# Performance work log

Hardware: AMD Instinct MI355X
Metric: run time of the kernel (lower is better)

Reference implementation:

```python
import jax, jax.numpy as jnp
import numpy as np

B, L, E = 8, 2048, 4096
TOKEN_DIM, EDGE_DIM, HIDDEN = 768, 256, 128


def setup_inputs() -> dict:
    key = jax.random.key(0)
    k1, k2, k3, k4, k5 = jax.random.split(key, 5)
    token_embedding = jax.random.normal(k1, (B, L, TOKEN_DIM), dtype=jnp.float32)
    edge_embedding = jax.random.normal(k2, (B, E, EDGE_DIM), dtype=jnp.float32)
    # fc: Linear(token_dim+edge_dim -> hidden, bias=False); stored as [in, out]
    W_fc = jax.random.normal(k3, (TOKEN_DIM + EDGE_DIM, HIDDEN), dtype=jnp.float32) * 0.02
    # attn_fc: Linear(2*hidden -> 1); weight flattened to [2*hidden], plus scalar bias
    a_attn = jax.random.normal(k4, (2 * HIDDEN,), dtype=jnp.float32) * 0.02
    b_attn = jax.random.normal(k5, (1,), dtype=jnp.float32) * 0.02
    return {"token_embedding": token_embedding, "edge_embedding": edge_embedding,
            "W_fc": W_fc, "a_attn": a_attn, "b_attn": b_attn}


def reference(token_embedding, edge_embedding, W_fc, a_attn, b_attn):
    # avg edge embedding, broadcast over sequence
    avg_edge = edge_embedding.mean(axis=1, keepdims=True)          # [B, 1, De]
    avg_edge = jnp.broadcast_to(avg_edge, (token_embedding.shape[0],
                                           token_embedding.shape[1],
                                           avg_edge.shape[-1]))     # [B, L, De]
    combined = jnp.concatenate([token_embedding, avg_edge], axis=-1)  # [B, L, Dt+De]
    h = jnp.einsum('bld,dh->blh', combined, W_fc)                   # [B, L, H]

    # Additive attention decomposition: a^T [h_j || h_i] = a1.h_j + a2.h_i
    # (original builds concat([h_repeat_row (=h_j), h_repeat_col (=h_i)]))
    H = h.shape[-1]
    a1, a2 = a_attn[:H], a_attn[H:]
    s_j = jnp.einsum('blh,h->bl', h, a1)                            # score contrib from h_j
    s_i = jnp.einsum('blh,h->bl', h, a2)                            # score contrib from h_i
    scores = s_i[:, :, None] + s_j[:, None, :] + b_attn[0]          # [B, L, L], scores[b,i,j]
    attn = jax.nn.softmax(scores, axis=-1)                          # softmax over j
    h_prime = jnp.einsum('bij,bjh->bih', attn, h)                   # [B, L, H]
    return h_prime
```

## Files before the change

kernel.cpp:

```cpp
#include <hip/hip_runtime.h>

constexpr int Bn  = 8;
constexpr int Ln  = 2048;
constexpr int En  = 4096;
constexpr int TDn = 768;
constexpr int EDn = 256;
constexpr int Hn  = 128;

constexpr int OFF_V1    = 0;
constexpr int OFF_DEN   = 768;
constexpr int OFF_T     = 1024;
constexpr int OFF_ES    = 8192;
constexpr int OFF_ROW   = 10240;
constexpr int OFF_EPART = 16384;
constexpr int OFF_TPART = 278528;
constexpr int REC = 772;

__global__ __launch_bounds__(256)
void K_init(const float* __restrict__ W, const float* __restrict__ a,
            float* __restrict__ ws) {
    const int tid = threadIdx.x, wv = tid >> 6, lane = tid & 63;
    int d = blockIdx.x * 4 + wv;
    float acc = W[d * Hn + lane]      * a[lane]
              + W[d * Hn + 64 + lane] * a[64 + lane];
    #pragma unroll
    for (int off = 32; off > 0; off >>= 1)
        acc += __shfl_down(acc, off, 64);
    if (lane == 0) ws[OFF_V1 + d] = acc;
}

__global__ __launch_bounds__(256)
void K_main(const float* __restrict__ token, const float* __restrict__ edge,
            float* __restrict__ ws) {
    const int tid = threadIdx.x, wv = tid >> 6, lane = tid & 63;
    __shared__ float4 s_red[4][64];
    __shared__ float4 s_v1[TDn / 4];
    __shared__ float  s_s[16];
    __shared__ float  s_e[16];

    if (blockIdx.x < 1024) {
        int eb = blockIdx.x;
        int b = eb >> 7, chunk = eb & 127;
        const float4* e4 = (const float4*)edge
                         + ((size_t)(b * En + chunk * 32 + wv * 8)) * (EDn / 4) + lane;
        float4 acc = {0.f, 0.f, 0.f, 0.f};
        #pragma unroll
        for (int i = 0; i < 8; ++i) {
            float4 v = e4[(size_t)i * (EDn / 4)];
            acc.x += v.x; acc.y += v.y; acc.z += v.z; acc.w += v.w;
        }
        s_red[wv][lane] = acc;
        __syncthreads();
        if (tid < 64) {
            float4 r0 = s_red[0][tid], r1 = s_red[1][tid],
                   r2 = s_red[2][tid], r3 = s_red[3][tid];
            float4 s = {r0.x + r1.x + r2.x + r3.x, r0.y + r1.y + r2.y + r3.y,
                        r0.z + r1.z + r2.z + r3.z, r0.w + r1.w + r2.w + r3.w};
            ((float4*)(ws + OFF_EPART))[eb * 64 + tid] = s;
        }
        return;
    }

    int tb = blockIdx.x - 1024;
    const int b = tb >> 7, chunk = tb & 127;
    const size_t row0 = (size_t)(b * Ln + chunk * 16);

    if (tid < TDn / 4) s_v1[tid] = ((const float4*)(ws + OFF_V1))[tid];
    __syncthreads();

    #pragma unroll
    for (int i = 0; i < 4; ++i) {
        int li = wv * 4 + i;
        const float4* t4 = (const float4*)token + (row0 + li) * (TDn / 4);
        float acc = 0.f;
        #pragma unroll
        for (int j = 0; j < 3; ++j) {
            float4 t = t4[lane + 64 * j];
            float4 v = s_v1[lane + 64 * j];
            acc += t.x * v.x + t.y * v.y + t.z * v.z + t.w * v.w;
        }
        #pragma unroll
        for (int off = 32; off > 0; off >>= 1)
            acc += __shfl_down(acc, off, 64);
        if (lane == 0) s_s[li] = acc;
    }
    __syncthreads();

    if (tid < 16) s_e[tid] = expf(s_s[tid]);
    __syncthreads();

    float sum = 0.f;
    #pragma unroll
    for (int l = 0; l < 16; ++l) sum += s_e[l];

    const float* tok = token + row0 * TDn;
    float a0 = 0.f, a1 = 0.f, a2 = 0.f;
    #pragma unroll 4
    for (int l = 0; l < 16; ++l) {
        float e = s_e[l];
        const float* r = tok + (size_t)l * TDn;
        a0 += e * r[tid];
        a1 += e * r[tid + 256];
        a2 += e * r[tid + 512];
    }
    float* rec = ws + OFF_TPART + (size_t)tb * REC;
    if (tid == 0) rec[0] = sum;
    rec[4 + tid]       = a0;
    rec[4 + tid + 256] = a1;
    rec[4 + tid + 512] = a2;
}

__global__ __launch_bounds__(256)
void K2(float* __restrict__ ws) {
    const int tid = threadIdx.x;
    if (blockIdx.x < 24) {
        int b = blockIdx.x / 3, part = blockIdx.x % 3;
        const float* recs = ws + OFF_TPART + (size_t)(b * 128) * REC + 4 + part * 256;
        float acc = 0.f;
        #pragma unroll 4
        for (int k = 0; k < 128; ++k) acc += recs[(size_t)k * REC + tid];
        ws[OFF_T + b * TDn + part * 256 + tid] = acc;
    } else {
        int b = blockIdx.x - 24;
        const float* p = ws + OFF_EPART + (size_t)(b * 128) * EDn + tid;
        float acc = 0.f;
        #pragma unroll 4
        for (int k = 0; k < 128; ++k) acc += p[(size_t)k * EDn];
        ws[OFF_ES + b * EDn + tid] = acc * (1.0f / En);

        __shared__ float s_red[128];
        if (tid < 128)
            s_red[tid] = ws[OFF_TPART + (size_t)(b * 128 + tid) * REC];
        __syncthreads();
        if (tid < 64)  { s_red[tid] += s_red[tid + 64]; } __syncthreads();
        if (tid < 32)  { s_red[tid] += s_red[tid + 32]; } __syncthreads();
        if (tid < 16)  { s_red[tid] += s_red[tid + 16]; } __syncthreads();
        if (tid == 0) {
            float d = 0.f;
            #pragma unroll
            for (int i = 0; i < 16; ++i) d += s_red[i];
            ws[OFF_DEN + b] = d;
        }
    }
}

__global__ __launch_bounds__(256)
void K3(const float* __restrict__ W, float* __restrict__ ws) {
    __shared__ float s_c[1024];
    __shared__ float s_red[256];
    const int b = blockIdx.x >> 3, hg = blockIdx.x & 7;
    const int tid = threadIdx.x;
    const int hidx = tid & 15, dseg = tid >> 4;
    const int h = hg * 16 + hidx;

    float invden = 1.0f / ws[OFF_DEN + b];
    #pragma unroll
    for (int k = 0; k < 4; ++k) {
        int i = tid + k * 256;
        s_c[i] = (i < TDn) ? ws[OFF_T + b * TDn + i] * invden
                           : ws[OFF_ES + b * EDn + (i - TDn)];
    }
    __syncthreads();

    const float* w = W + (dseg * 64) * Hn + h;
    float acc = 0.f;
    #pragma unroll 4
    for (int i = 0; i < 64; ++i)
        acc += s_c[dseg * 64 + i] * w[i * Hn];
    s_red[tid] = acc;
    __syncthreads();
    if (tid < 16) {
        float r = 0.f;
        #pragma unroll
        for (int g = 0; g < 16; ++g) r += s_red[g * 16 + tid];
        ws[OFF_ROW + b * Hn + hg * 16 + tid] = r;
    }
}

__global__ __launch_bounds__(256)
void K4(const float* __restrict__ ws, float4* __restrict__ out) {
    int idx = blockIdx.x * blockDim.x + threadIdx.x;
    int b = idx >> 16;
    int q = idx & (Hn / 4 - 1);
    out[idx] = ((const float4*)(ws + OFF_ROW))[b * (Hn / 4) + q];
}

extern "C" void kernel_launch(void* const* d_in, const int* in_sizes, int n_in,
                              void* d_out, int out_size, void* d_ws, size_t ws_size,
                              hipStream_t stream) {
    const float* token = (const float*)d_in[0];
    const float* edge  = (const float*)d_in[1];
    const float* W     = (const float*)d_in[2];
    const float* a     = (const float*)d_in[3];
    float* ws  = (float*)d_ws;
    float4* out = (float4*)d_out;

    K_init<<<192,  256, 0, stream>>>(W, a, ws);
    K_main<<<2048, 256, 0, stream>>>(token, edge, ws);
    K2    <<<32,   256, 0, stream>>>(ws);
    K3    <<<64,   256, 0, stream>>>(W, ws);
    K4    <<<2048, 256, 0, stream>>>(ws, out);
}
```

Baseline: 138.0 us.

## Fuse all stages into one cooperative kernel with grid-wide syncs

Replaces the five separate kernel launches with a single cooperative kernel of 1024 blocks that runs each stage in turn, separated by grid.sync(). Each block now handles both an edge chunk and a token chunk, and the output broadcast writes two float4 per thread. The aim is to remove launch overhead and inter-kernel gaps. In exchange it adds grid-barrier cost, and stages that only use a few blocks leave most of the grid idle. It falls back to the old multi-kernel path if the cooperative launch fails.

```diff
diff --git a/kernel.cpp b/kernel.cpp
--- a/kernel.cpp
+++ b/kernel.cpp
@@ -1,4 +1,7 @@
 #include <hip/hip_runtime.h>
+#include <hip/hip_cooperative_groups.h>
+
+namespace cg = cooperative_groups;
 
 constexpr int Bn  = 8;
 constexpr int Ln  = 2048;
@@ -15,6 +18,173 @@
 constexpr int OFF_EPART = 16384;
 constexpr int OFF_TPART = 278528;
 constexpr int REC = 772;
+
+__global__ __launch_bounds__(256, 4)
+void K_all(const float* __restrict__ token, const float* __restrict__ edge,
+           const float* __restrict__ W, const float* __restrict__ a,
+           float* __restrict__ ws, float4* __restrict__ out)
+{
+    cg::grid_group grid = cg::this_grid();
+    const int tid = threadIdx.x, wv = tid >> 6, lane = tid & 63;
+    const int bi = blockIdx.x;
+
+    __shared__ __align__(16) float sm[2048];
+
+    if (bi < 192) {
+        int d = bi * 4 + wv;
+        float acc = W[d * Hn + lane]      * a[lane]
+                  + W[d * Hn + 64 + lane] * a[64 + lane];
+        #pragma unroll
+        for (int off = 32; off > 0; off >>= 1)
+            acc += __shfl_down(acc, off, 64);
+        if (lane == 0) ws[OFF_V1 + d] = acc;
+    }
+    grid.sync();
+
+    {
+        const int b = bi >> 7, chunk = bi & 127;
+
+        const float4* e4 = (const float4*)edge
+                         + ((size_t)(b * En + chunk * 32 + wv * 8)) * (EDn / 4) + lane;
+        float4 acc = {0.f, 0.f, 0.f, 0.f};
+        #pragma unroll
+        for (int i = 0; i < 8; ++i) {
+            float4 v = e4[(size_t)i * (EDn / 4)];
+            acc.x += v.x; acc.y += v.y; acc.z += v.z; acc.w += v.w;
+        }
+        float4* RED = (float4*)(sm + 768);
+        RED[wv * 64 + lane] = acc;
+        __syncthreads();
+        if (tid < 64) {
+            float4 r0 = RED[tid], r1 = RED[64 + tid],
+                   r2 = RED[128 + tid], r3 = RED[192 + tid];
+            float4 s = {r0.x + r1.x + r2.x + r3.x, r0.y + r1.y + r2.y + r3.y,
+                        r0.z + r1.z + r2.z + r3.z, r0.w + r1.w + r2.w + r3.w};
+            ((float4*)(ws + OFF_EPART))[bi * 64 + tid] = s;
+        }
+
+        float4* V1 = (float4*)sm;
+        if (tid < TDn / 4) V1[tid] = ((const float4*)(ws + OFF_V1))[tid];
+        __syncthreads();
+
+        const size_t row0 = (size_t)(b * Ln + chunk * 16);
+        float* s_s = sm + 1792;
+        float* s_e = sm + 1808;
+
+        #pragma unroll
+        for (int i = 0; i < 4; ++i) {
+            int li = wv * 4 + i;
+            const float4* t4 = (const float4*)token + (row0 + li) * (TDn / 4);
+            float acc2 = 0.f;
+            #pragma unroll
+            for (int j = 0; j < 3; ++j) {
+                float4 t = t4[lane + 64 * j];
+                float4 v = V1[lane + 64 * j];
+                acc2 += t.x * v.x + t.y * v.y + t.z * v.z + t.w * v.w;
+            }
+            #pragma unroll
+            for (int off = 32; off > 0; off >>= 1)
+                acc2 += __shfl_down(acc2, off, 64);
+            if (lane == 0) s_s[li] = acc2;
+        }
+        __syncthreads();
+        if (tid < 16) s_e[tid] = expf(s_s[tid]);
+        __syncthreads();
+
+        float sum = 0.f;
+        #pragma unroll
+        for (int l = 0; l < 16; ++l) sum += s_e[l];
+
+        const float* tok = token + row0 * TDn;
+        float a0 = 0.f, a1 = 0.f, a2 = 0.f;
+        #pragma unroll 4
+        for (int l = 0; l < 16; ++l) {
+            float e = s_e[l];
+            const float* r = tok + (size_t)l * TDn;
+            a0 += e * r[tid];
+            a1 += e * r[tid + 256];
+            a2 += e * r[tid + 512];
+        }
+        float* rec = ws + OFF_TPART + (size_t)bi * REC;
+        if (tid == 0) rec[0] = sum;
+        rec[4 + tid]       = a0;
+        rec[4 + tid + 256] = a1;
+        rec[4 + tid + 512] = a2;
+    }
+    grid.sync();
+
+    if (bi < 32) {
+        if (bi < 24) {
+            int b = bi / 3, part = bi % 3;
+            const float* recs = ws + OFF_TPART + (size_t)(b * 128) * REC + 4 + part * 256;
+            float acc = 0.f;
+            #pragma unroll 4
+            for (int k = 0; k < 128; ++k) acc += recs[(size_t)k * REC + tid];
+            ws[OFF_T + b * TDn + part * 256 + tid] = acc;
+        } else {
+            int b = bi - 24;
+            const float* p = ws + OFF_EPART + (size_t)(b * 128) * EDn + tid;
+            float acc = 0.f;
+            #pragma unroll 4
+            for (int k = 0; k < 128; ++k) acc += p[(size_t)k * EDn];
+            ws[OFF_ES + b * EDn + tid] = acc * (1.0f / En);
+
+            if (tid < 128)
+                sm[tid] = ws[OFF_TPART + (size_t)(b * 128 + tid) * REC];
+            __syncthreads();
+            if (tid < 64)  { sm[tid] += sm[tid + 64]; } __syncthreads();
+            if (tid < 32)  { sm[tid] += sm[tid + 32]; } __syncthreads();
+            if (tid < 16)  { sm[tid] += sm[tid + 16]; } __syncthreads();
+            if (tid == 0) {
+                float d = 0.f;
+                #pragma unroll
+                for (int i = 0; i < 16; ++i) d += sm[i];
+                ws[OFF_DEN + b] = d;
+            }
+        }
+    }
+    grid.sync();
+
+    if (bi < 64) {
+        float* s_c  = sm;
+        float* s_rd = sm + 1024;
+        const int b = bi >> 3, hg = bi & 7;
+        const int hidx = tid & 15, dseg = tid >> 4;
+        const int h = hg * 16 + hidx;
+
+        float invden = 1.0f / ws[OFF_DEN + b];
+        #pragma unroll
+        for (int k = 0; k < 4; ++k) {
+            int i = tid + k * 256;
+            s_c[i] = (i < TDn) ? ws[OFF_T + b * TDn + i] * invden
+                               : ws[OFF_ES + b * EDn + (i - TDn)];
+        }
+        __syncthreads();
+
+        const float* w = W + (dseg * 64) * Hn + h;
+        float acc = 0.f;
+        #pragma unroll 4
+        for (int i = 0; i < 64; ++i)
+            acc += s_c[dseg * 64 + i] * w[i * Hn];
+        s_rd[tid] = acc;
+        __syncthreads();
+        if (tid < 16) {
+            float r = 0.f;
+            #pragma unroll
+            for (int g = 0; g < 16; ++g) r += s_rd[g * 16 + tid];
+            ws[OFF_ROW + b * Hn + hg * 16 + tid] = r;
+        }
+    }
+    grid.sync();
+
+    {
+        const float4* row4 = (const float4*)(ws + OFF_ROW);
+        int i0 = bi * 512 + tid;
+        out[i0] = row4[(i0 >> 16) * (Hn / 4) + (i0 & (Hn / 4 - 1))];
+        int i1 = i0 + 256;
+        out[i1] = row4[(i1 >> 16) * (Hn / 4) + (i1 & (Hn / 4 - 1))];
+    }
+}
 
 __global__ __launch_bounds__(256)
 void K_init(const float* __restrict__ W, const float* __restrict__ a,
@@ -192,12 +362,18 @@
     const float* edge  = (const float*)d_in[1];
     const float* W     = (const float*)d_in[2];
     const float* a     = (const float*)d_in[3];
-    float* ws  = (float*)d_ws;
+    float* ws   = (float*)d_ws;
     float4* out = (float4*)d_out;
 
-    K_init<<<192,  256, 0, stream>>>(W, a, ws);
-    K_main<<<2048, 256, 0, stream>>>(token, edge, ws);
-    K2    <<<32,   256, 0, stream>>>(ws);
-    K3    <<<64,   256, 0, stream>>>(W, ws);
-    K4    <<<2048, 256, 0, stream>>>(ws, out);
-}
+    void* args[6] = {(void*)&token, (void*)&edge, (void*)&W, (void*)&a,
+                     (void*)&ws, (void*)&out};
+    hipError_t err = hipLaunchCooperativeKernel(K_all, dim3(1024), dim3(256),
+                                                args, 0u, stream);
+    if (err != hipSuccess) {
+        K_init<<<192,  256, 0, stream>>>(W, a, ws);
+        K_main<<<2048, 256, 0, stream>>>(token, edge, ws);
+        K2    <<<32,   256, 0, stream>>>(ws);
+        K3    <<<64,   256, 0, stream>>>(W, ws);
+        K4    <<<2048, 256, 0, stream>>>(ws, out);
+    }
+}
```

Result: slower. 505.6 us (+266.4%).

## Fuse five launches into two, recomputing projection vectors per block

Applied to the files above, without the earlier changes.

Folds the W·a projection into the token-scoring blocks, so every token block recomputes the 768-length vector from W and a in shared memory. The per-batch reductions, the small GEMV and the broadcast write are merged into one second kernel. In that kernel each of 32 slices per batch redundantly re-reduces the partials before writing its share of the output. Token blocks now cover 32 rows instead of 16, halving the partial records. This removes three launches and their inter-kernel gaps, at the cost of much redundant L2 traffic from re-reading W and the partials in every block.

```diff
diff --git a/kernel.cpp b/kernel.cpp
--- a/kernel.cpp
+++ b/kernel.cpp
@@ -7,36 +7,17 @@
 constexpr int EDn = 256;
 constexpr int Hn  = 128;
 
-constexpr int OFF_V1    = 0;
-constexpr int OFF_DEN   = 768;
-constexpr int OFF_T     = 1024;
-constexpr int OFF_ES    = 8192;
-constexpr int OFF_ROW   = 10240;
 constexpr int OFF_EPART = 16384;
 constexpr int OFF_TPART = 278528;
 constexpr int REC = 772;
 
 __global__ __launch_bounds__(256)
-void K_init(const float* __restrict__ W, const float* __restrict__ a,
-            float* __restrict__ ws) {
+void K_1(const float* __restrict__ token, const float* __restrict__ edge,
+         const float* __restrict__ W, const float* __restrict__ a,
+         float* __restrict__ ws)
+{
     const int tid = threadIdx.x, wv = tid >> 6, lane = tid & 63;
-    int d = blockIdx.x * 4 + wv;
-    float acc = W[d * Hn + lane]      * a[lane]
-              + W[d * Hn + 64 + lane] * a[64 + lane];
-    #pragma unroll
-    for (int off = 32; off > 0; off >>= 1)
-        acc += __shfl_down(acc, off, 64);
-    if (lane == 0) ws[OFF_V1 + d] = acc;
-}
-
-__global__ __launch_bounds__(256)
-void K_main(const float* __restrict__ token, const float* __restrict__ edge,
-            float* __restrict__ ws) {
-    const int tid = threadIdx.x, wv = tid >> 6, lane = tid & 63;
-    __shared__ float4 s_red[4][64];
-    __shared__ float4 s_v1[TDn / 4];
-    __shared__ float  s_s[16];
-    __shared__ float  s_e[16];
+    __shared__ __align__(16) float sm[2048];
 
     if (blockIdx.x < 1024) {
         int eb = blockIdx.x;
@@ -49,11 +30,12 @@
             float4 v = e4[(size_t)i * (EDn / 4)];
             acc.x += v.x; acc.y += v.y; acc.z += v.z; acc.w += v.w;
         }
-        s_red[wv][lane] = acc;
+        float4* RED = (float4*)(sm + 768);
+        RED[wv * 64 + lane] = acc;
         __syncthreads();
         if (tid < 64) {
-            float4 r0 = s_red[0][tid], r1 = s_red[1][tid],
-                   r2 = s_red[2][tid], r3 = s_red[3][tid];
+            float4 r0 = RED[tid], r1 = RED[64 + tid],
+                   r2 = RED[128 + tid], r3 = RED[192 + tid];
             float4 s = {r0.x + r1.x + r2.x + r3.x, r0.y + r1.y + r2.y + r3.y,
                         r0.z + r1.z + r2.z + r3.z, r0.w + r1.w + r2.w + r3.w};
             ((float4*)(ws + OFF_EPART))[eb * 64 + tid] = s;
@@ -61,42 +43,59 @@
         return;
     }
 
-    int tb = blockIdx.x - 1024;
-    const int b = tb >> 7, chunk = tb & 127;
-    const size_t row0 = (size_t)(b * Ln + chunk * 16);
+    const int tb = blockIdx.x - 1024;
+    const int b = tb >> 6, chunk = tb & 63;
+    const size_t row0 = (size_t)(b * Ln + chunk * 32);
 
-    if (tid < TDn / 4) s_v1[tid] = ((const float4*)(ws + OFF_V1))[tid];
+    if (tid < 32) ((float4*)(sm + 1024))[tid] = ((const float4*)a)[tid];
+    __syncthreads();
+    const float4* av = (const float4*)(sm + 1024);
+    #pragma unroll
+    for (int r = 0; r < 3; ++r) {
+        int d = tid + r * 256;
+        const float4* w4 = (const float4*)(W + (size_t)d * Hn);
+        float acc = 0.f;
+        #pragma unroll 8
+        for (int j = 0; j < 32; ++j) {
+            float4 w = w4[j], aa = av[j];
+            acc += w.x * aa.x + w.y * aa.y + w.z * aa.z + w.w * aa.w;
+        }
+        sm[d] = acc;
+    }
     __syncthreads();
 
+    const float4* V1 = (const float4*)sm;
+    float* s_s = sm + 1792;
+    float* s_e = sm + 1824;
+
     #pragma unroll
-    for (int i = 0; i < 4; ++i) {
-        int li = wv * 4 + i;
+    for (int i = 0; i < 8; ++i) {
+        int li = wv * 8 + i;
         const float4* t4 = (const float4*)token + (row0 + li) * (TDn / 4);
-        float acc = 0.f;
+        float acc2 = 0.f;
         #pragma unroll
         for (int j = 0; j < 3; ++j) {
             float4 t = t4[lane + 64 * j];
-            float4 v = s_v1[lane + 64 * j];
-            acc += t.x * v.x + t.y * v.y + t.z * v.z + t.w * v.w;
+            float4 v = V1[lane + 64 * j];
+            acc2 += t.x * v.x + t.y * v.y + t.z * v.z + t.w * v.w;
         }
         #pragma unroll
         for (int off = 32; off > 0; off >>= 1)
-            acc += __shfl_down(acc, off, 64);
-        if (lane == 0) s_s[li] = acc;
+            acc2 += __shfl_down(acc2, off, 64);
+        if (lane == 0) s_s[li] = acc2;
     }
     __syncthreads();
-
-    if (tid < 16) s_e[tid] = expf(s_s[tid]);
+    if (tid < 32) s_e[tid] = expf(s_s[tid]);
     __syncthreads();
 
     float sum = 0.f;
     #pragma unroll
-    for (int l = 0; l < 16; ++l) sum += s_e[l];
+    for (int l = 0; l < 32; ++l) sum += s_e[l];
 
     const float* tok = token + row0 * TDn;
     float a0 = 0.f, a1 = 0.f, a2 = 0.f;
     #pragma unroll 4
-    for (int l = 0; l < 16; ++l) {
+    for (int l = 0; l < 32; ++l) {
         float e = s_e[l];
         const float* r = tok + (size_t)l * TDn;
         a0 += e * r[tid];
@@ -111,78 +110,65 @@
 }
 
 __global__ __launch_bounds__(256)
-void K2(float* __restrict__ ws) {
-    const int tid = threadIdx.x;
-    if (blockIdx.x < 24) {
-        int b = blockIdx.x / 3, part = blockIdx.x % 3;
-        const float* recs = ws + OFF_TPART + (size_t)(b * 128) * REC + 4 + part * 256;
-        float acc = 0.f;
-        #pragma unroll 4
-        for (int k = 0; k < 128; ++k) acc += recs[(size_t)k * REC + tid];
-        ws[OFF_T + b * TDn + part * 256 + tid] = acc;
-    } else {
-        int b = blockIdx.x - 24;
-        const float* p = ws + OFF_EPART + (size_t)(b * 128) * EDn + tid;
-        float acc = 0.f;
-        #pragma unroll 4
-        for (int k = 0; k < 128; ++k) acc += p[(size_t)k * EDn];
-        ws[OFF_ES + b * EDn + tid] = acc * (1.0f / En);
-
-        __shared__ float s_red[128];
-        if (tid < 128)
-            s_red[tid] = ws[OFF_TPART + (size_t)(b * 128 + tid) * REC];
-        __syncthreads();
-        if (tid < 64)  { s_red[tid] += s_red[tid + 64]; } __syncthreads();
-        if (tid < 32)  { s_red[tid] += s_red[tid + 32]; } __syncthreads();
-        if (tid < 16)  { s_red[tid] += s_red[tid + 16]; } __syncthreads();
-        if (tid == 0) {
-            float d = 0.f;
-            #pragma unroll
-            for (int i = 0; i < 16; ++i) d += s_red[i];
-            ws[OFF_DEN + b] = d;
-        }
-    }
-}
-
-__global__ __launch_bounds__(256)
-void K3(const float* __restrict__ W, float* __restrict__ ws) {
+void K_2(const float* __restrict__ W, float* __restrict__ ws,
+         float4* __restrict__ out)
+{
     __shared__ float s_c[1024];
     __shared__ float s_red[256];
-    const int b = blockIdx.x >> 3, hg = blockIdx.x & 7;
+    __shared__ float s_row[128];
+    __shared__ float s_den;
     const int tid = threadIdx.x;
-    const int hidx = tid & 15, dseg = tid >> 4;
-    const int h = hg * 16 + hidx;
+    const int b = blockIdx.x >> 5, slice = blockIdx.x & 31;
 
-    float invden = 1.0f / ws[OFF_DEN + b];
-    #pragma unroll
-    for (int k = 0; k < 4; ++k) {
-        int i = tid + k * 256;
-        s_c[i] = (i < TDn) ? ws[OFF_T + b * TDn + i] * invden
-                           : ws[OFF_ES + b * EDn + (i - TDn)];
+    const float* recs = ws + OFF_TPART + (size_t)(b * 64) * REC;
+    float t0 = 0.f, t1 = 0.f, t2 = 0.f;
+    #pragma unroll 4
+    for (int k = 0; k < 64; ++k) {
+        const float* r = recs + (size_t)k * REC + 4;
+        t0 += r[tid];
+        t1 += r[tid + 256];
+        t2 += r[tid + 512];
     }
+
+    if (tid < 64) {
+        float dv = recs[(size_t)tid * REC];
+        #pragma unroll
+        for (int off = 32; off > 0; off >>= 1)
+            dv += __shfl_down(dv, off, 64);
+        if (tid == 0) s_den = dv;
+    }
+
+    const float* ep = ws + OFF_EPART + (size_t)(b * 128) * EDn + tid;
+    float ev = 0.f;
+    #pragma unroll 4
+    for (int k = 0; k < 128; ++k) ev += ep[(size_t)k * EDn];
+
+    __syncthreads();
+    float invden = 1.0f / s_den;
+    s_c[tid]       = t0 * invden;
+    s_c[tid + 256] = t1 * invden;
+    s_c[tid + 512] = t2 * invden;
+    s_c[768 + tid] = ev * (1.0f / En);
     __syncthreads();
 
-    const float* w = W + (dseg * 64) * Hn + h;
+    const int h = tid & 127, half = tid >> 7;
+    const float* w = W + (size_t)(half * 512) * Hn + h;
     float acc = 0.f;
-    #pragma unroll 4
-    for (int i = 0; i < 64; ++i)
-        acc += s_c[dseg * 64 + i] * w[i * Hn];
+    #pragma unroll 8
+    for (int i = 0; i < 512; ++i)
+        acc += s_c[half * 512 + i] * w[(size_t)i * Hn];
     s_red[tid] = acc;
     __syncthreads();
-    if (tid < 16) {
-        float r = 0.f;
-        #pragma unroll
-        for (int g = 0; g < 16; ++g) r += s_red[g * 16 + tid];
-        ws[OFF_ROW + b * Hn + hg * 16 + tid] = r;
+    if (tid < 128) s_row[tid] = s_red[tid] + s_red[tid + 128];
+    __syncthreads();
+
+    const float4* r4 = (const float4*)s_row;
+    float4* ob = out + ((size_t)(b * Ln + slice * 64)) * (Hn / 4);
+    #pragma unroll
+    for (int k = 0; k < 8; ++k) {
+        int f = k * 256 + tid;
+        ob[f] = r4[f & 31];
     }
-}
-
-__global__ __launch_bounds__(256)
-void K4(const float* __restrict__ ws, float4* __restrict__ out) {
-    int idx = blockIdx.x * blockDim.x + threadIdx.x;
-    int b = idx >> 16;
-    int q = idx & (Hn / 4 - 1);
-    out[idx] = ((const float4*)(ws + OFF_ROW))[b * (Hn / 4) + q];
 }
 
 extern "C" void kernel_launch(void* const* d_in, const int* in_sizes, int n_in,
@@ -192,12 +178,9 @@
     const float* edge  = (const float*)d_in[1];
     const float* W     = (const float*)d_in[2];
     const float* a     = (const float*)d_in[3];
-    float* ws  = (float*)d_ws;
+    float* ws   = (float*)d_ws;
     float4* out = (float4*)d_out;
 
-    K_init<<<192,  256, 0, stream>>>(W, a, ws);
-    K_main<<<2048, 256, 0, stream>>>(token, edge, ws);
-    K2    <<<32,   256, 0, stream>>>(ws);
-    K3    <<<64,   256, 0, stream>>>(W, ws);
-    K4    <<<2048, 256, 0, stream>>>(ws, out);
+    K_1<<<1536, 256, 0, stream>>>(token, edge, W, a, ws);
+    K_2<<<256,  256, 0, stream>>>(W, ws, out);
 }
```

Measured after the change: 173.8 us. +26.0%, slower.
